# Kernel tuning notes

Hardware: AMD Instinct MI355X
Metric: run time of the kernel (lower is better)

Reference implementation:

```python
import jax, jax.numpy as jnp
import numpy as np

NU, NI, K, D, B = 100000, 50000, 100, 64, 8192


def setup_inputs() -> dict:
    key = jax.random.key(0)
    ks = jax.random.split(key, 16)
    s = lambda fan_in: np.sqrt(2.0 / fan_in)  # kaiming_normal-ish scale
    return {
        "user_emb": jax.random.normal(ks[0], (NU, D), jnp.float32) * s(D),
        "item_emb": jax.random.normal(ks[1], (NI, D), jnp.float32) * s(D),
        "user_scr_tensor": jax.random.uniform(ks[2], (NU, K), jnp.float32) / K,
        "item_scr_tensor": jax.random.uniform(ks[3], (NI, K), jnp.float32) / K,
        "w1": jax.random.normal(ks[4], (64, 128), jnp.float32) * s(128),
        "b1": jnp.zeros((64,), jnp.float32),
        "w2": jax.random.normal(ks[5], (64, 64), jnp.float32) * s(64),
        "b2": jnp.zeros((64,), jnp.float32),
        "w3": jax.random.normal(ks[6], (32, 64), jnp.float32) * s(64),
        "b3": jnp.zeros((32,), jnp.float32),
        "w4": jax.random.normal(ks[7], (32, 32), jnp.float32) * s(32),
        "b4": jnp.zeros((32,), jnp.float32),
        "w5": jax.random.normal(ks[8], (1, 32), jnp.float32) * s(32),
        "b5": jnp.zeros((1,), jnp.float32),
        "user_idx_tensor": jax.random.randint(ks[9], (NU, K), 0, NU, jnp.int32),
        "item_idx_tensor": jax.random.randint(ks[10], (NI, K), 0, NI, jnp.int32),
        "user_idxs": jax.random.randint(ks[11], (B,), 0, NU, jnp.int32),
        "item_idxs": jax.random.randint(ks[12], (B,), 0, NI, jnp.int32),
    }


def _scored_pool(idx_tensor, emb, scr, idxs):
    neighs = idx_tensor[idxs]          # [B, K]
    neigh_emb = emb[neighs]            # [B, K, D]
    neigh_scr = scr[neighs]            # [B, K, K]
    return jnp.einsum("bkj,bjd->bkd", neigh_scr, neigh_emb)


def reference(user_emb, item_emb, user_scr_tensor, item_scr_tensor,
              w1, b1, w2, b2, w3, b3, w4, b4, w5, b5,
              user_idx_tensor, item_idx_tensor, user_idxs, item_idxs):
    su = _scored_pool(user_idx_tensor, user_emb, user_scr_tensor, user_idxs)  # [B,K,D]
    si = _scored_pool(item_idx_tensor, item_emb, item_scr_tensor, item_idxs)  # [B,K,D]
    x = jnp.concatenate([su, si], axis=2)  # [B, K, 2D]
    x = jax.nn.relu(x @ w1.T + b1)
    x = jax.nn.relu(x @ w2.T + b2)
    x = jax.nn.relu(x @ w3.T + b3)
    x = jax.nn.relu(x @ w4.T + b4)
    x = jax.nn.sigmoid(x @ w5.T + b5)  # [B, K, 1]
    return jnp.mean(x, axis=-2).squeeze()  # [B]
```

## Files before the change

### kernel.cpp

```cpp
#include <hip/hip_runtime.h>
#include <hip/hip_bf16.h>
#include <math.h>

typedef __attribute__((ext_vector_type(8))) short short8;
typedef __attribute__((ext_vector_type(4))) float f32x4;

#define KN 100

#define W1_OFF 0
#define W2_OFF 8192
#define W3_OFF 12288
#define W4_OFF 14336
#define SCRU_OFF 16384
#define SCRI_OFF (SCRU_OFF + 100000 * 128)
#define EMBU_OFF (SCRI_OFF + 50000 * 128)
#define EMBI_OFF (EMBU_OFF + 100000 * 64)

#define ET_OFF 0
#define XU_OFF (64 * 136)
#define XI_OFF (XU_OFF + 112 * 72)
#define S_TOT  (XI_OFF + 112 * 72)

__device__ __forceinline__ unsigned short f2bf(float f) {
  __hip_bfloat16 h = __float2bfloat16(f);
  return __builtin_bit_cast(unsigned short, h);
}

__device__ __forceinline__ void st8(unsigned short* d, float4 a, float4 b) {
  short8 h;
  h[0] = (short)f2bf(a.x); h[1] = (short)f2bf(a.y);
  h[2] = (short)f2bf(a.z); h[3] = (short)f2bf(a.w);
  h[4] = (short)f2bf(b.x); h[5] = (short)f2bf(b.y);
  h[6] = (short)f2bf(b.z); h[7] = (short)f2bf(b.w);
  *reinterpret_cast<short8*>(d) = h;
}

__global__ void prep(const float* __restrict__ w1, const float* __restrict__ w2,
                     const float* __restrict__ w3, const float* __restrict__ w4,
                     const float* __restrict__ uscr, const float* __restrict__ iscr,
                     const float* __restrict__ uemb, const float* __restrict__ iemb,
                     unsigned short* __restrict__ ws) {
  int t = blockIdx.x * 256 + threadIdx.x;
  if (t < 15360) {
    const float* src; int rel, o, i, kt, base;
    if (t < 8192)       { src = w1; rel = t;         o = rel >> 7; i = rel & 127; kt = 4; base = W1_OFF; }
    else if (t < 12288) { src = w2; rel = t - 8192;  o = rel >> 6; i = rel & 63;  kt = 2; base = W2_OFF; }
    else if (t < 14336) { src = w3; rel = t - 12288; o = rel >> 6; i = rel & 63;  kt = 2; base = W3_OFF; }
    else                { src = w4; rel = t - 14336; o = rel >> 5; i = rel & 31;  kt = 1; base = W4_OFF; }
    int n = o >> 4, l15 = o & 15, k = i >> 5, quad = (i >> 3) & 3, j = i & 7;
    ws[base + ((n * kt + k) * 64 + quad * 16 + l15) * 8 + j] = f2bf(src[rel]);
    return;
  }
  int rel = t - 15360;
  const float4 z4 = {0.f, 0.f, 0.f, 0.f};
  if (rel < 2400000) {
    const float* src; unsigned short* dst; int row, g;
    if (rel < 1600000) {
      row = rel >> 4; g = rel & 15;
      src = uscr + (size_t)row * 100;
      dst = ws + SCRU_OFF + (size_t)row * 128 + g * 8;
    } else {
      int q = rel - 1600000; row = q >> 4; g = q & 15;
      src = iscr + (size_t)row * 100;
      dst = ws + SCRI_OFF + (size_t)row * 128 + g * 8;
    }
    float4 va = (g < 13) ? *reinterpret_cast<const float4*>(src + g * 8) : z4;
    float4 vb = (g < 12) ? *reinterpret_cast<const float4*>(src + g * 8 + 4) : z4;
    st8(dst, va, vb);
    return;
  }
  rel -= 2400000;
  if (rel < 1200000) {
    const float* src; unsigned short* dst; int row, g;
    if (rel < 800000) {
      row = rel >> 3; g = rel & 7;
      src = uemb + (size_t)row * 64;
      dst = ws + EMBU_OFF + (size_t)row * 64 + g * 8;
    } else {
      int q = rel - 800000; row = q >> 3; g = q & 7;
      src = iemb + (size_t)row * 64;
      dst = ws + EMBI_OFF + (size_t)row * 64 + g * 8;
    }
    float4 va = *reinterpret_cast<const float4*>(src + g * 8);
    float4 vb = *reinterpret_cast<const float4*>(src + g * 8 + 4);
    st8(dst, va, vb);
  }
}

template <int NT, int KT, bool RELU>
__device__ __forceinline__ void mlp_layer(const short8* a,
                                          const unsigned short* __restrict__ gw,
                                          const float* __restrict__ bias,
                                          unsigned short* __restrict__ Y, int sY,
                                          int w, int l15, int quad, int lane) {
#pragma unroll
  for (int n = 0; n < NT; ++n) {
    f32x4 acc = {0.f, 0.f, 0.f, 0.f};
#pragma unroll
    for (int k = 0; k < KT; ++k) {
      short8 bf = *reinterpret_cast<const short8*>(gw + ((n * KT + k) * 64 + lane) * 8);
      acc = __builtin_amdgcn_mfma_f32_16x16x32_bf16(a[k], bf, acc, 0, 0, 0);
    }
    const int col = n * 16 + l15;
    const float bv = bias[col];
#pragma unroll
    for (int r = 0; r < 4; ++r) {
      float v = acc[r] + bv;
      if (RELU) v = fmaxf(v, 0.f);
      Y[(w * 16 + quad * 4 + r) * sY + col] = f2bf(v);
    }
  }
}

__launch_bounds__(448)
__global__ void cnn_mfma3(
    const unsigned short* __restrict__ ws,
    const float* __restrict__ b1, const float* __restrict__ b2,
    const float* __restrict__ b3, const float* __restrict__ b4,
    const float* __restrict__ w5, const float* __restrict__ b5,
    const int* __restrict__ user_idx_t, const int* __restrict__ item_idx_t,
    const int* __restrict__ user_idxs, const int* __restrict__ item_idxs,
    float* __restrict__ out) {
  __shared__ __align__(16) unsigned short S[S_TOT];
  __shared__ int s_nb[2][112];
  __shared__ float s_red[7];

  const int b = blockIdx.x;
  const int tid = threadIdx.x;
  const int w = tid >> 6;
  const int lane = tid & 63;
  const int l15 = lane & 15, quad = lane >> 4;

  if (tid < 112) {
    s_nb[0][tid] = (tid < KN) ? user_idx_t[(size_t)user_idxs[b] * KN + tid] : 0;
  } else if (tid >= 128 && tid < 240) {
    int i = tid - 128;
    s_nb[1][i] = (i < KN) ? item_idx_t[(size_t)item_idxs[b] * KN + i] : 0;
  }
  {
    int* z = (int*)S;
    for (int i = tid; i < (64 * 136) / 2; i += 448) z[i] = 0;
  }
  __syncthreads();

  const int mrow = w * 16 + l15;
  const int c = lane & 31, half = lane >> 5;

#pragma unroll 1
  for (int src = 0; src < 2; ++src) {
    const unsigned short* scrb = ws + (src ? SCRI_OFF : SCRU_OFF);
    const unsigned short* embb = ws + (src ? EMBI_OFF : EMBU_OFF);
    const int* nb = s_nb[src];

    short8 a[4];
    {
      const unsigned short* arow = scrb + (size_t)nb[mrow] * 128;
#pragma unroll
      for (int k = 0; k < 4; ++k)
        a[k] = *reinterpret_cast<const short8*>(arow + k * 32 + quad * 8);
    }

#pragma unroll
    for (int rr = 0; rr < 8; ++rr) {
      const int rbase = w + rr * 7;
      if (rbase < 50) {
        const int r = rbase * 2 + half;
        unsigned int v = *reinterpret_cast<const unsigned int*>(
            embb + (size_t)nb[r] * 64 + c * 2);
        S[ET_OFF + (2 * c) * 136 + r] = (unsigned short)(v & 0xffffu);
        S[ET_OFF + (2 * c + 1) * 136 + r] = (unsigned short)(v >> 16);
      }
    }
    __syncthreads();

    const int xoff = src ? XI_OFF : XU_OFF;
#pragma unroll
    for (int n = 0; n < 4; ++n) {
      f32x4 acc = {0.f, 0.f, 0.f, 0.f};
#pragma unroll
      for (int k = 0; k < 4; ++k) {
        short8 bf = *reinterpret_cast<const short8*>(
            S + ET_OFF + (n * 16 + l15) * 136 + k * 32 + quad * 8);
        acc = __builtin_amdgcn_mfma_f32_16x16x32_bf16(a[k], bf, acc, 0, 0, 0);
      }
#pragma unroll
      for (int r = 0; r < 4; ++r)
        S[xoff + (w * 16 + quad * 4 + r) * 72 + n * 16 + l15] = f2bf(acc[r]);
    }
    if (src == 0) __syncthreads();
  }

  {
    short8 a[4];
    a[0] = *reinterpret_cast<const short8*>(S + XU_OFF + (w * 16 + l15) * 72 + quad * 8);
    a[1] = *reinterpret_cast<const short8*>(S + XU_OFF + (w * 16 + l15) * 72 + 32 + quad * 8);
    a[2] = *reinterpret_cast<const short8*>(S + XI_OFF + (w * 16 + l15) * 72 + quad * 8);
    a[3] = *reinterpret_cast<const short8*>(S + XI_OFF + (w * 16 + l15) * 72 + 32 + quad * 8);
    mlp_layer<4, 4, true>(a, ws + W1_OFF, b1, S + XU_OFF, 72, w, l15, quad, lane);
  }
  {
    short8 a[2];
    a[0] = *reinterpret_cast<const short8*>(S + XU_OFF + (w * 16 + l15) * 72 + quad * 8);
    a[1] = *reinterpret_cast<const short8*>(S + XU_OFF + (w * 16 + l15) * 72 + 32 + quad * 8);
    mlp_layer<4, 2, true>(a, ws + W2_OFF, b2, S + XI_OFF, 72, w, l15, quad, lane);
  }
  {
    short8 a[2];
    a[0] = *reinterpret_cast<const short8*>(S + XI_OFF + (w * 16 + l15) * 72 + quad * 8);
    a[1] = *reinterpret_cast<const short8*>(S + XI_OFF + (w * 16 + l15) * 72 + 32 + quad * 8);
    mlp_layer<2, 2, true>(a, ws + W3_OFF, b3, S + XU_OFF, 72, w, l15, quad, lane);
  }
  {
    short8 a = *reinterpret_cast<const short8*>(S + XU_OFF + (w * 16 + l15) * 72 + quad * 8);
    float dot[4] = {0.f, 0.f, 0.f, 0.f};
#pragma unroll
    for (int n = 0; n < 2; ++n) {
      f32x4 acc = {0.f, 0.f, 0.f, 0.f};
      short8 bf = *reinterpret_cast<const short8*>(ws + W4_OFF + (n * 64 + lane) * 8);
      acc = __builtin_amdgcn_mfma_f32_16x16x32_bf16(a, bf, acc, 0, 0, 0);
      const int col = n * 16 + l15;
      const float bv = b4[col], wv = w5[col];
#pragma unroll
      for (int r = 0; r < 4; ++r) {
        float v = fmaxf(acc[r] + bv, 0.f);
        dot[r] = fmaf(v, wv, dot[r]);
      }
    }
    float wsum = 0.f;
    const float bb5 = b5[0];
#pragma unroll
    for (int r = 0; r < 4; ++r) {
      float s = dot[r];
      s += __shfl_xor(s, 1, 64);
      s += __shfl_xor(s, 2, 64);
      s += __shfl_xor(s, 4, 64);
      s += __shfl_xor(s, 8, 64);
      const int row = w * 16 + quad * 4 + r;
      if (l15 == 0 && row < KN) wsum += 1.f / (1.f + expf(-(s + bb5)));
    }
    wsum += __shfl_xor(wsum, 16, 64);
    wsum += __shfl_xor(wsum, 32, 64);
    if (lane == 0) s_red[w] = wsum;
  }
  __syncthreads();
  if (tid == 0) {
    float t = 0.f;
#pragma unroll
    for (int i = 0; i < 7; ++i) t += s_red[i];
    out[b] = t * (1.0f / KN);
  }
}

extern "C" void kernel_launch(void* const* d_in, const int* in_sizes, int n_in,
                              void* d_out, int out_size, void* d_ws,
                              size_t ws_size, hipStream_t stream) {
  const float* user_emb = (const float*)d_in[0];
  const float* item_emb = (const float*)d_in[1];
  const float* user_scr = (const float*)d_in[2];
  const float* item_scr = (const float*)d_in[3];
  const float* w1 = (const float*)d_in[4];
  const float* b1 = (const float*)d_in[5];
  const float* w2 = (const float*)d_in[6];
  const float* b2 = (const float*)d_in[7];
  const float* w3 = (const float*)d_in[8];
  const float* b3 = (const float*)d_in[9];
  const float* w4 = (const float*)d_in[10];
  const float* b4 = (const float*)d_in[11];
  const float* w5 = (const float*)d_in[12];
  const float* b5 = (const float*)d_in[13];
  const int* user_idx_t = (const int*)d_in[14];
  const int* item_idx_t = (const int*)d_in[15];
  const int* user_idxs = (const int*)d_in[16];
  const int* item_idxs = (const int*)d_in[17];
  unsigned short* wsw = (unsigned short*)d_ws;

  prep<<<dim3((15360 + 2400000 + 1200000 + 255) / 256), dim3(256), 0, stream>>>(
      w1, w2, w3, w4, user_scr, item_scr, user_emb, item_emb, wsw);

  const int B = in_sizes[16];
  cnn_mfma3<<<dim3(B), dim3(448), 0, stream>>>(
      wsw, b1, b2, b3, b4, w5, b5, user_idx_t, item_idx_t, user_idxs,
      item_idxs, (float*)d_out);
}
```

Baseline: 378.1 us.

## Keep MLP activations in registers via transposed MFMA with permuted K layout

The pooling and MLP layers are recomputed in transposed form (weights as the A operand, activations as B), and the K dimension of weights, score rows and embedding columns is permuted so each MFMA output accumulator can be packed straight into the next layer's B fragment. All inter-layer LDS round-trips and most block barriers go away, LDS shrinks to the single embedding-transpose buffer, and the final reduction is simplified. The cost is a more intricate index permutation in prep and in the embedding scatter, and higher register pressure from keeping several accumulators live.

```diff
diff --git a/kernel.cpp b/kernel.cpp
--- a/kernel.cpp
+++ b/kernel.cpp
@@ -16,10 +16,8 @@
 #define EMBU_OFF (SCRI_OFF + 50000 * 128)
 #define EMBI_OFF (EMBU_OFF + 100000 * 64)
 
-#define ET_OFF 0
-#define XU_OFF (64 * 136)
-#define XI_OFF (XU_OFF + 112 * 72)
-#define S_TOT  (XI_OFF + 112 * 72)
+#define ET_STRIDE 136
+#define S_TOT (64 * ET_STRIDE)
 
 __device__ __forceinline__ unsigned short f2bf(float f) {
   __hip_bfloat16 h = __float2bfloat16(f);
@@ -33,6 +31,15 @@
   h[4] = (short)f2bf(b.x); h[5] = (short)f2bf(b.y);
   h[6] = (short)f2bf(b.z); h[7] = (short)f2bf(b.w);
   *reinterpret_cast<short8*>(d) = h;
+}
+
+__device__ __forceinline__ short8 pk2(f32x4 a, f32x4 b) {
+  short8 h;
+  h[0] = (short)f2bf(a[0]); h[1] = (short)f2bf(a[1]);
+  h[2] = (short)f2bf(a[2]); h[3] = (short)f2bf(a[3]);
+  h[4] = (short)f2bf(b[0]); h[5] = (short)f2bf(b[1]);
+  h[6] = (short)f2bf(b[2]); h[7] = (short)f2bf(b[3]);
+  return h;
 }
 
 __global__ void prep(const float* __restrict__ w1, const float* __restrict__ w2,
@@ -47,8 +54,9 @@
     else if (t < 12288) { src = w2; rel = t - 8192;  o = rel >> 6; i = rel & 63;  kt = 2; base = W2_OFF; }
     else if (t < 14336) { src = w3; rel = t - 12288; o = rel >> 6; i = rel & 63;  kt = 2; base = W3_OFF; }
     else                { src = w4; rel = t - 14336; o = rel >> 5; i = rel & 31;  kt = 1; base = W4_OFF; }
-    int n = o >> 4, l15 = o & 15, k = i >> 5, quad = (i >> 3) & 3, j = i & 7;
-    ws[base + ((n * kt + k) * 64 + quad * 16 + l15) * 8 + j] = f2bf(src[rel]);
+    int n = o >> 4, l15 = o & 15, k = i >> 5;
+    int quad = (i >> 2) & 3, s = ((i >> 4) & 1) * 4 + (i & 3);
+    ws[base + ((n * kt + k) * 64 + quad * 16 + l15) * 8 + s] = f2bf(src[rel]);
     return;
   }
   int rel = t - 15360;
@@ -64,8 +72,9 @@
       src = iscr + (size_t)row * 100;
       dst = ws + SCRI_OFF + (size_t)row * 128 + g * 8;
     }
-    float4 va = (g < 13) ? *reinterpret_cast<const float4*>(src + g * 8) : z4;
-    float4 vb = (g < 12) ? *reinterpret_cast<const float4*>(src + g * 8 + 4) : z4;
+    const int jb = 32 * (g >> 2) + 4 * (g & 3);
+    float4 va = (jb <= 96) ? *reinterpret_cast<const float4*>(src + jb) : z4;
+    float4 vb = (jb <= 80) ? *reinterpret_cast<const float4*>(src + jb + 16) : z4;
     st8(dst, va, vb);
     return;
   }
@@ -87,33 +96,50 @@
   }
 }
 
-template <int NT, int KT, bool RELU>
-__device__ __forceinline__ void mlp_layer(const short8* a,
-                                          const unsigned short* __restrict__ gw,
-                                          const float* __restrict__ bias,
-                                          unsigned short* __restrict__ Y, int sY,
-                                          int w, int l15, int quad, int lane) {
-#pragma unroll
-  for (int n = 0; n < NT; ++n) {
-    f32x4 acc = {0.f, 0.f, 0.f, 0.f};
-#pragma unroll
-    for (int k = 0; k < KT; ++k) {
-      short8 bf = *reinterpret_cast<const short8*>(gw + ((n * KT + k) * 64 + lane) * 8);
-      acc = __builtin_amdgcn_mfma_f32_16x16x32_bf16(a[k], bf, acc, 0, 0, 0);
-    }
-    const int col = n * 16 + l15;
-    const float bv = bias[col];
-#pragma unroll
-    for (int r = 0; r < 4; ++r) {
-      float v = acc[r] + bv;
-      if (RELU) v = fmaxf(v, 0.f);
-      Y[(w * 16 + quad * 4 + r) * sY + col] = f2bf(v);
-    }
-  }
+__device__ __forceinline__ void pool_one(
+    const unsigned short* __restrict__ scrb, const unsigned short* __restrict__ embb,
+    const int* __restrict__ nb, unsigned short* __restrict__ S,
+    int w, int l15, int quad, int c, int half, int mrow, bool bar_after,
+    short8& f0, short8& f1) {
+  short8 sb[4];
+  const unsigned short* arow = scrb + (size_t)nb[mrow] * 128;
+#pragma unroll
+  for (int k = 0; k < 4; ++k)
+    sb[k] = *reinterpret_cast<const short8*>(arow + k * 32 + quad * 8);
+
+#pragma unroll
+  for (int rr = 0; rr < 8; ++rr) {
+    const int rbase = w + rr * 7;
+    if (rbase < 50) {
+      const int r = rbase * 2 + half;
+      unsigned int v = *reinterpret_cast<const unsigned int*>(
+          embb + (size_t)nb[r] * 64 + c * 2);
+      const int p = 32 * (r >> 5) + 8 * ((r >> 2) & 3) + 4 * ((r >> 4) & 1) + (r & 3);
+      S[(2 * c) * ET_STRIDE + p] = (unsigned short)(v & 0xffffu);
+      S[(2 * c + 1) * ET_STRIDE + p] = (unsigned short)(v >> 16);
+    }
+  }
+  __syncthreads();
+
+  f32x4 acc[4];
+#pragma unroll
+  for (int po = 0; po < 4; ++po) acc[po] = (f32x4){0.f, 0.f, 0.f, 0.f};
+#pragma unroll
+  for (int k4 = 0; k4 < 4; ++k4) {
+#pragma unroll
+    for (int po = 0; po < 4; ++po) {
+      short8 ea = *reinterpret_cast<const short8*>(
+          S + (po * 16 + l15) * ET_STRIDE + k4 * 32 + quad * 8);
+      acc[po] = __builtin_amdgcn_mfma_f32_16x16x32_bf16(ea, sb[k4], acc[po], 0, 0, 0);
+    }
+  }
+  if (bar_after) __syncthreads();
+  f0 = pk2(acc[0], acc[1]);
+  f1 = pk2(acc[2], acc[3]);
 }
 
 __launch_bounds__(448)
-__global__ void cnn_mfma3(
+__global__ void cnn_mfma4(
     const unsigned short* __restrict__ ws,
     const float* __restrict__ b1, const float* __restrict__ b2,
     const float* __restrict__ b3, const float* __restrict__ b4,
@@ -139,115 +165,115 @@
   }
   {
     int* z = (int*)S;
-    for (int i = tid; i < (64 * 136) / 2; i += 448) z[i] = 0;
+    for (int i = tid; i < S_TOT / 2; i += 448) z[i] = 0;
   }
   __syncthreads();
 
   const int mrow = w * 16 + l15;
   const int c = lane & 31, half = lane >> 5;
 
-#pragma unroll 1
-  for (int src = 0; src < 2; ++src) {
-    const unsigned short* scrb = ws + (src ? SCRI_OFF : SCRU_OFF);
-    const unsigned short* embb = ws + (src ? EMBI_OFF : EMBU_OFF);
-    const int* nb = s_nb[src];
-
-    short8 a[4];
-    {
-      const unsigned short* arow = scrb + (size_t)nb[mrow] * 128;
-#pragma unroll
-      for (int k = 0; k < 4; ++k)
-        a[k] = *reinterpret_cast<const short8*>(arow + k * 32 + quad * 8);
-    }
-
-#pragma unroll
-    for (int rr = 0; rr < 8; ++rr) {
-      const int rbase = w + rr * 7;
-      if (rbase < 50) {
-        const int r = rbase * 2 + half;
-        unsigned int v = *reinterpret_cast<const unsigned int*>(
-            embb + (size_t)nb[r] * 64 + c * 2);
-        S[ET_OFF + (2 * c) * 136 + r] = (unsigned short)(v & 0xffffu);
-        S[ET_OFF + (2 * c + 1) * 136 + r] = (unsigned short)(v >> 16);
+  short8 x0, x1, x2, x3;
+  pool_one(ws + SCRU_OFF, ws + EMBU_OFF, s_nb[0], S, w, l15, quad, c, half, mrow,
+           true, x0, x1);
+  pool_one(ws + SCRI_OFF, ws + EMBI_OFF, s_nb[1], S, w, l15, quad, c, half, mrow,
+           false, x2, x3);
+
+  f32x4 y[4];
+#pragma unroll
+  for (int po = 0; po < 4; ++po) y[po] = (f32x4){0.f, 0.f, 0.f, 0.f};
+  {
+    short8 xf[4] = {x0, x1, x2, x3};
+#pragma unroll
+    for (int k4 = 0; k4 < 4; ++k4)
+#pragma unroll
+      for (int po = 0; po < 4; ++po) {
+        short8 wa = *reinterpret_cast<const short8*>(
+            ws + W1_OFF + ((po * 4 + k4) * 64 + lane) * 8);
+        y[po] = __builtin_amdgcn_mfma_f32_16x16x32_bf16(wa, xf[k4], y[po], 0, 0, 0);
       }
-    }
-    __syncthreads();
-
-    const int xoff = src ? XI_OFF : XU_OFF;
-#pragma unroll
-    for (int n = 0; n < 4; ++n) {
-      f32x4 acc = {0.f, 0.f, 0.f, 0.f};
-#pragma unroll
-      for (int k = 0; k < 4; ++k) {
-        short8 bf = *reinterpret_cast<const short8*>(
-            S + ET_OFF + (n * 16 + l15) * 136 + k * 32 + quad * 8);
-        acc = __builtin_amdgcn_mfma_f32_16x16x32_bf16(a[k], bf, acc, 0, 0, 0);
-      }
-#pragma unroll
-      for (int r = 0; r < 4; ++r)
-        S[xoff + (w * 16 + quad * 4 + r) * 72 + n * 16 + l15] = f2bf(acc[r]);
-    }
-    if (src == 0) __syncthreads();
-  }
-
-  {
-    short8 a[4];
-    a[0] = *reinterpret_cast<const short8*>(S + XU_OFF + (w * 16 + l15) * 72 + quad * 8);
-    a[1] = *reinterpret_cast<const short8*>(S + XU_OFF + (w * 16 + l15) * 72 + 32 + quad * 8);
-    a[2] = *reinterpret_cast<const short8*>(S + XI_OFF + (w * 16 + l15) * 72 + quad * 8);
-    a[3] = *reinterpret_cast<const short8*>(S + XI_OFF + (w * 16 + l15) * 72 + 32 + quad * 8);
-    mlp_layer<4, 4, true>(a, ws + W1_OFF, b1, S + XU_OFF, 72, w, l15, quad, lane);
-  }
-  {
-    short8 a[2];
-    a[0] = *reinterpret_cast<const short8*>(S + XU_OFF + (w * 16 + l15) * 72 + quad * 8);
-    a[1] = *reinterpret_cast<const short8*>(S + XU_OFF + (w * 16 + l15) * 72 + 32 + quad * 8);
-    mlp_layer<4, 2, true>(a, ws + W2_OFF, b2, S + XI_OFF, 72, w, l15, quad, lane);
-  }
-  {
-    short8 a[2];
-    a[0] = *reinterpret_cast<const short8*>(S + XI_OFF + (w * 16 + l15) * 72 + quad * 8);
-    a[1] = *reinterpret_cast<const short8*>(S + XI_OFF + (w * 16 + l15) * 72 + 32 + quad * 8);
-    mlp_layer<2, 2, true>(a, ws + W3_OFF, b3, S + XU_OFF, 72, w, l15, quad, lane);
-  }
-  {
-    short8 a = *reinterpret_cast<const short8*>(S + XU_OFF + (w * 16 + l15) * 72 + quad * 8);
-    float dot[4] = {0.f, 0.f, 0.f, 0.f};
-#pragma unroll
-    for (int n = 0; n < 2; ++n) {
-      f32x4 acc = {0.f, 0.f, 0.f, 0.f};
-      short8 bf = *reinterpret_cast<const short8*>(ws + W4_OFF + (n * 64 + lane) * 8);
-      acc = __builtin_amdgcn_mfma_f32_16x16x32_bf16(a, bf, acc, 0, 0, 0);
-      const int col = n * 16 + l15;
-      const float bv = b4[col], wv = w5[col];
-#pragma unroll
-      for (int r = 0; r < 4; ++r) {
-        float v = fmaxf(acc[r] + bv, 0.f);
-        dot[r] = fmaf(v, wv, dot[r]);
-      }
-    }
-    float wsum = 0.f;
-    const float bb5 = b5[0];
-#pragma unroll
-    for (int r = 0; r < 4; ++r) {
-      float s = dot[r];
-      s += __shfl_xor(s, 1, 64);
-      s += __shfl_xor(s, 2, 64);
-      s += __shfl_xor(s, 4, 64);
-      s += __shfl_xor(s, 8, 64);
-      const int row = w * 16 + quad * 4 + r;
-      if (l15 == 0 && row < KN) wsum += 1.f / (1.f + expf(-(s + bb5)));
-    }
-    wsum += __shfl_xor(wsum, 16, 64);
-    wsum += __shfl_xor(wsum, 32, 64);
-    if (lane == 0) s_red[w] = wsum;
-  }
+  }
+#pragma unroll
+  for (int po = 0; po < 4; ++po) {
+    const float4 bb = *reinterpret_cast<const float4*>(b1 + po * 16 + quad * 4);
+#pragma unroll
+    for (int r = 0; r < 4; ++r) y[po][r] = fmaxf(y[po][r] + bb[r], 0.f);
+  }
+  short8 g0 = pk2(y[0], y[1]), g1 = pk2(y[2], y[3]);
+
+  f32x4 v[4];
+#pragma unroll
+  for (int po = 0; po < 4; ++po) v[po] = (f32x4){0.f, 0.f, 0.f, 0.f};
+#pragma unroll
+  for (int k4 = 0; k4 < 2; ++k4) {
+    short8 gf = k4 ? g1 : g0;
+#pragma unroll
+    for (int po = 0; po < 4; ++po) {
+      short8 wa = *reinterpret_cast<const short8*>(
+          ws + W2_OFF + ((po * 2 + k4) * 64 + lane) * 8);
+      v[po] = __builtin_amdgcn_mfma_f32_16x16x32_bf16(wa, gf, v[po], 0, 0, 0);
+    }
+  }
+#pragma unroll
+  for (int po = 0; po < 4; ++po) {
+    const float4 bb = *reinterpret_cast<const float4*>(b2 + po * 16 + quad * 4);
+#pragma unroll
+    for (int r = 0; r < 4; ++r) v[po][r] = fmaxf(v[po][r] + bb[r], 0.f);
+  }
+  short8 h0 = pk2(v[0], v[1]), h1 = pk2(v[2], v[3]);
+
+  f32x4 t3[2];
+  t3[0] = (f32x4){0.f, 0.f, 0.f, 0.f};
+  t3[1] = (f32x4){0.f, 0.f, 0.f, 0.f};
+#pragma unroll
+  for (int k4 = 0; k4 < 2; ++k4) {
+    short8 gf = k4 ? h1 : h0;
+#pragma unroll
+    for (int po = 0; po < 2; ++po) {
+      short8 wa = *reinterpret_cast<const short8*>(
+          ws + W3_OFF + ((po * 2 + k4) * 64 + lane) * 8);
+      t3[po] = __builtin_amdgcn_mfma_f32_16x16x32_bf16(wa, gf, t3[po], 0, 0, 0);
+    }
+  }
+#pragma unroll
+  for (int po = 0; po < 2; ++po) {
+    const float4 bb = *reinterpret_cast<const float4*>(b3 + po * 16 + quad * 4);
+#pragma unroll
+    for (int r = 0; r < 4; ++r) t3[po][r] = fmaxf(t3[po][r] + bb[r], 0.f);
+  }
+  short8 q0 = pk2(t3[0], t3[1]);
+
+  f32x4 u[2];
+  u[0] = (f32x4){0.f, 0.f, 0.f, 0.f};
+  u[1] = (f32x4){0.f, 0.f, 0.f, 0.f};
+#pragma unroll
+  for (int po = 0; po < 2; ++po) {
+    short8 wa = *reinterpret_cast<const short8*>(ws + W4_OFF + (po * 64 + lane) * 8);
+    u[po] = __builtin_amdgcn_mfma_f32_16x16x32_bf16(wa, q0, u[po], 0, 0, 0);
+  }
+  float part = 0.f;
+#pragma unroll
+  for (int po = 0; po < 2; ++po) {
+    const float4 bb = *reinterpret_cast<const float4*>(b4 + po * 16 + quad * 4);
+    const float4 wv = *reinterpret_cast<const float4*>(w5 + po * 16 + quad * 4);
+#pragma unroll
+    for (int r = 0; r < 4; ++r)
+      part = fmaf(fmaxf(u[po][r] + bb[r], 0.f), wv[r], part);
+  }
+  part += __shfl_xor(part, 16, 64);
+  part += __shfl_xor(part, 32, 64);
+  float sig = 1.f / (1.f + expf(-(part + b5[0])));
+  if (mrow >= KN) sig = 0.f;
+  sig += __shfl_xor(sig, 1, 64);
+  sig += __shfl_xor(sig, 2, 64);
+  sig += __shfl_xor(sig, 4, 64);
+  sig += __shfl_xor(sig, 8, 64);
+  if (lane == 0) s_red[w] = sig;
   __syncthreads();
   if (tid == 0) {
-    float t = 0.f;
-#pragma unroll
-    for (int i = 0; i < 7; ++i) t += s_red[i];
-    out[b] = t * (1.0f / KN);
+    float acc = 0.f;
+#pragma unroll
+    for (int i = 0; i < 7; ++i) acc += s_red[i];
+    out[b] = acc * (1.0f / KN);
   }
 }
 
@@ -278,7 +304,7 @@
       w1, w2, w3, w4, user_scr, item_scr, user_emb, item_emb, wsw);
 
   const int B = in_sizes[16];
-  cnn_mfma3<<<dim3(B), dim3(448), 0, stream>>>(
+  cnn_mfma4<<<dim3(B), dim3(448), 0, stream>>>(
       wsw, b1, b2, b3, b4, w5, b5, user_idx_t, item_idx_t, user_idxs,
       item_idxs, (float*)d_out);
 }
```

New measurement: 385.3 us. No clear change (+1.9%).
